# Kernel tuning notes

Hardware: AMD Instinct MI355X
Metric: run time of the kernel (lower is better)

## Reference

```python
import jax, jax.numpy as jnp
import numpy as np

N_SENT = 262144
N_BAGS = 4096
HIDDEN = 256
HIER = 2
LAYER0 = 14
NUM_CLASSES = 53


def setup_inputs() -> dict:
    key = jax.random.key(0)
    ks = jax.random.split(key, 8)
    x = jax.random.normal(ks[0], (N_SENT, HIDDEN), dtype=jnp.float32)
    rel_emb0 = jax.random.normal(ks[1], (LAYER0, HIDDEN), dtype=jnp.float32) * 0.1
    rel_emb1 = jax.random.normal(ks[2], (NUM_CLASSES, HIDDEN), dtype=jnp.float32) * 0.1
    disc = jax.random.normal(ks[3], (NUM_CLASSES, 2 * HIDDEN), dtype=jnp.float32) * 0.05
    bias = jnp.zeros((NUM_CLASSES,), dtype=jnp.float32)
    # relation_levels[r] = (coarse node id, fine node id) for relation r
    relation_levels = jnp.stack(
        [jax.random.randint(ks[4], (NUM_CLASSES,), 0, LAYER0, dtype=jnp.int32),
         jnp.arange(NUM_CLASSES, dtype=jnp.int32)], axis=1)
    label_index = jax.random.randint(ks[5], (N_SENT,), 0, NUM_CLASSES, dtype=jnp.int32)
    # ragged bag boundaries: scope[0]=0, scope[-1]=N_SENT, interior sorted
    interior = jnp.sort(jax.random.randint(ks[6], (N_BAGS - 1,), 1, N_SENT, dtype=jnp.int32))
    scope = jnp.concatenate([jnp.zeros((1,), jnp.int32), interior,
                             jnp.full((1,), N_SENT, jnp.int32)])
    return {"x": x, "rel_emb0": rel_emb0, "rel_emb1": rel_emb1, "disc": disc,
            "bias": bias, "relation_levels": relation_levels,
            "label_index": label_index, "scope": scope}


def _segment_ids(scope, n):
    # scope: [B+1] sorted boundaries -> per-sentence bag id [n]
    marks = jnp.zeros((n,), jnp.int32).at[scope[1:-1]].add(1)
    return jnp.cumsum(marks)


def reference(x, rel_emb0, rel_emb1, disc, bias, relation_levels, label_index, scope):
    n = x.shape[0]
    b = scope.shape[0] - 1
    seg = _segment_ids(scope, n)                       # [N]
    ll = relation_levels[label_index]                  # [N, 2]
    # per-level attention logits: <rel_emb[level][node], x>
    lg0 = jnp.sum(rel_emb0[ll[:, 0]] * x, axis=-1)     # [N]
    lg1 = jnp.sum(rel_emb1[ll[:, 1]] * x, axis=-1)     # [N]
    logits = jnp.stack([lg0, lg1], axis=1)             # [N, hier]
    # ragged softmax per bag (stable)
    m = jax.ops.segment_max(logits, seg, num_segments=b)     # [B, hier]
    e = jnp.exp(logits - m[seg])
    s = jax.ops.segment_sum(e, seg, num_segments=b)          # [B, hier]
    score = e / s[seg]                                       # [N, hier]
    # attention-weighted sentence reduction per bag per level
    weighted = score[:, :, None] * x[:, None, :]             # [N, hier, H]
    repre = jax.ops.segment_sum(weighted, seg, num_segments=b)  # [B, hier, H]
    stack_repre = repre.reshape(b, HIER * HIDDEN)            # [B, 2H]
    return stack_repre @ disc.T + bias                       # [B, 53]
```

## Files before the change

### kernel.cpp

```cpp
#include <hip/hip_runtime.h>
#include <math.h>

#define HIDDEN 256
#define NUM_CLASSES 53
#define NWAVES 4
#define BLOCK (NWAVES * 64)
#define KP 4

template <int CTRL>
__device__ __forceinline__ float dpp_add(float v) {
    int t = __builtin_amdgcn_update_dpp(0, __float_as_int(v), CTRL, 0xf, 0xf, true);
    return v + __int_as_float(t);
}

__device__ __forceinline__ float wave_sum64(float v) {
    v = dpp_add<0x111>(v);
    v = dpp_add<0x112>(v);
    v = dpp_add<0x114>(v);
    v = dpp_add<0x118>(v);
    v = dpp_add<0x142>(v);
    v = dpp_add<0x143>(v);
    return __int_as_float(__builtin_amdgcn_readlane(__float_as_int(v), 63));
}

__global__ __launch_bounds__(BLOCK, 4) void hattn_fused_kernel(
    const float* __restrict__ x,
    const float* __restrict__ rel_emb0,
    const float* __restrict__ rel_emb1,
    const float* __restrict__ disc,
    const float* __restrict__ bias,
    const int* __restrict__ relation_levels,
    const int* __restrict__ label_index,
    const int* __restrict__ scope,
    float* __restrict__ out)
{
    const int bag   = blockIdx.x;
    const int start = scope[bag];
    const int end   = scope[bag + 1];

    const int tid  = threadIdx.x;
    const int lane = tid & 63;
    const int wave = tid >> 6;
    const int col  = lane << 2;

    float4 o0 = make_float4(0,0,0,0), o1 = make_float4(0,0,0,0);
    float  l0 = 0.f, l1 = 0.f;

    for (int rbase = start + wave * KP; rbase < end; rbase += NWAVES * KP) {
        const int nv = end - rbase;

        float4 xv[KP];
        int    lbl[KP];
        #pragma unroll
        for (int k = 0; k < KP; ++k) {
            const int rc = (k < nv) ? (rbase + k) : rbase;
            const int rcs = __builtin_amdgcn_readfirstlane(rc);
            xv[k]  = *reinterpret_cast<const float4*>(x + ((size_t)rcs << 8) + col);
            lbl[k] = label_index[rcs];
        }

        float e0[KP], e1[KP];
        #pragma unroll
        for (int k = 0; k < KP; ++k) {
            const int2 rl = *reinterpret_cast<const int2*>(relation_levels + 2 * lbl[k]);
            const float4 r0 = *reinterpret_cast<const float4*>(rel_emb0 + ((size_t)rl.x << 8) + col);
            const float4 r1 = *reinterpret_cast<const float4*>(rel_emb1 + ((size_t)rl.y << 8) + col);
            float p0 = xv[k].x*r0.x + xv[k].y*r0.y + xv[k].z*r0.z + xv[k].w*r0.w;
            float p1 = xv[k].x*r1.x + xv[k].y*r1.y + xv[k].z*r1.z + xv[k].w*r1.w;
            const float s0 = wave_sum64(p0);
            const float s1 = wave_sum64(p1);
            e0[k] = (k < nv) ? __expf(s0) : 0.f;
            e1[k] = (k < nv) ? __expf(s1) : 0.f;
        }

        #pragma unroll
        for (int k = 0; k < KP; ++k) {
            l0 += e0[k];
            l1 += e1[k];
            o0.x += e0[k]*xv[k].x; o0.y += e0[k]*xv[k].y; o0.z += e0[k]*xv[k].z; o0.w += e0[k]*xv[k].w;
            o1.x += e1[k]*xv[k].x; o1.y += e1[k]*xv[k].y; o1.z += e1[k]*xv[k].z; o1.w += e1[k]*xv[k].w;
        }
    }

    __shared__ alignas(16) float s_o[2][NWAVES][HIDDEN];
    __shared__ float s_l[NWAVES][2];
    __shared__ alignas(16) float s_repre[2 * HIDDEN];
    __shared__ float s_inv[2];

    *reinterpret_cast<float4*>(&s_o[0][wave][col]) = o0;
    *reinterpret_cast<float4*>(&s_o[1][wave][col]) = o1;
    if (lane == 0) { s_l[wave][0] = l0; s_l[wave][1] = l1; }
    __syncthreads();

    {
        const int t = tid;
        const float a0 = s_o[0][0][t] + s_o[0][1][t] + s_o[0][2][t] + s_o[0][3][t];
        const float a1 = s_o[1][0][t] + s_o[1][1][t] + s_o[1][2][t] + s_o[1][3][t];
        s_repre[t]          = a0;
        s_repre[HIDDEN + t] = a1;
        if (tid == 0) {
            const float L0 = s_l[0][0] + s_l[1][0] + s_l[2][0] + s_l[3][0];
            const float L1 = s_l[0][1] + s_l[1][1] + s_l[2][1] + s_l[3][1];
            s_inv[0] = (L0 > 0.f) ? 1.f / L0 : 0.f;
            s_inv[1] = (L1 > 0.f) ? 1.f / L1 : 0.f;
        }
    }
    __syncthreads();

    {
        const int c  = tid >> 2;
        const int l4 = tid & 3;
        if (c < NUM_CLASSES) {
            const float4* dr = reinterpret_cast<const float4*>(disc + (size_t)c * (2 * HIDDEN));
            const float4* rp = reinterpret_cast<const float4*>(s_repre);
            float pH0 = 0.f, pH1 = 0.f;
            #pragma unroll
            for (int i = 0; i < 16; ++i) {
                const int idx = l4 + 4 * i;
                const float4 a = rp[idx];
                const float4 d = dr[idx];
                pH0 += a.x*d.x + a.y*d.y + a.z*d.z + a.w*d.w;
            }
            #pragma unroll
            for (int i = 16; i < 32; ++i) {
                const int idx = l4 + 4 * i;
                const float4 a = rp[idx];
                const float4 d = dr[idx];
                pH1 += a.x*d.x + a.y*d.y + a.z*d.z + a.w*d.w;
            }
            float p = pH0 * s_inv[0] + pH1 * s_inv[1];
            p = dpp_add<0xB1>(p);
            p = dpp_add<0x4E>(p);
            if (l4 == 0) out[bag * NUM_CLASSES + c] = p + bias[c];
        }
    }
}

extern "C" void kernel_launch(void* const* d_in, const int* in_sizes, int n_in,
                              void* d_out, int out_size, void* d_ws, size_t ws_size,
                              hipStream_t stream) {
    const float* x               = (const float*)d_in[0];
    const float* rel_emb0        = (const float*)d_in[1];
    const float* rel_emb1        = (const float*)d_in[2];
    const float* disc            = (const float*)d_in[3];
    const float* bias            = (const float*)d_in[4];
    const int*   relation_levels = (const int*)d_in[5];
    const int*   label_index     = (const int*)d_in[6];
    const int*   scope           = (const int*)d_in[7];
    float*       out             = (float*)d_out;

    const int n_bags = in_sizes[7] - 1;

    hattn_fused_kernel<<<n_bags, BLOCK, 0, stream>>>(
        x, rel_emb0, rel_emb1, disc, bias, relation_levels, label_index, scope, out);
}
```

Measured before the change: 419.9 us.

## Stage sentence tiles in LDS and split logit and reduction work across waves

Each block now copies 64-row tiles of x into padded shared memory. It computes both level logits per row with four threads and a short DPP reduction, instead of a full 64-lane reduction per row. The weighted sum is then split so each wave owns one level and half the rows, which removes the per-row wave-wide reductions. The cost is about 66KB of LDS per block, which cuts occupancy, plus three barriers per tile.

```diff
diff --git a/kernel.cpp b/kernel.cpp
--- a/kernel.cpp
+++ b/kernel.cpp
@@ -4,8 +4,9 @@
 #define HIDDEN 256
 #define NUM_CLASSES 53
 #define NWAVES 4
-#define BLOCK (NWAVES * 64)
-#define KP 4
+#define BLOCK 256
+#define TILE 64
+#define XPAD 260
 
 template <int CTRL>
 __device__ __forceinline__ float dpp_add(float v) {
@@ -13,17 +14,7 @@
     return v + __int_as_float(t);
 }
 
-__device__ __forceinline__ float wave_sum64(float v) {
-    v = dpp_add<0x111>(v);
-    v = dpp_add<0x112>(v);
-    v = dpp_add<0x114>(v);
-    v = dpp_add<0x118>(v);
-    v = dpp_add<0x142>(v);
-    v = dpp_add<0x143>(v);
-    return __int_as_float(__builtin_amdgcn_readlane(__float_as_int(v), 63));
-}
-
-__global__ __launch_bounds__(BLOCK, 4) void hattn_fused_kernel(
+__global__ __launch_bounds__(BLOCK, 2) void hattn_tile_kernel(
     const float* __restrict__ x,
     const float* __restrict__ rel_emb0,
     const float* __restrict__ rel_emb1,
@@ -34,105 +25,138 @@
     const int* __restrict__ scope,
     float* __restrict__ out)
 {
+    __shared__ alignas(16) float s_x[TILE][XPAD];
+    __shared__ alignas(16) float s_e0[TILE];
+    __shared__ alignas(16) float s_e1[TILE];
+    __shared__ int2  s_rl[NUM_CLASSES];
+    __shared__ int2  s_rlc[TILE];
+    __shared__ float s_lw[NWAVES];
+    __shared__ alignas(16) float s_rep2[2][2][HIDDEN];
+
+    const int tid  = threadIdx.x;
+    const int lane = tid & 63;
+    const int wave = tid >> 6;
+
+    if (tid < NUM_CLASSES)
+        s_rl[tid] = *reinterpret_cast<const int2*>(relation_levels + 2 * tid);
+    {
+        float4 z = make_float4(0.f, 0.f, 0.f, 0.f);
+        float* base = &s_x[0][0];
+        const int nf4 = (TILE * XPAD) / 4;
+        for (int i = tid; i < nf4; i += BLOCK)
+            *reinterpret_cast<float4*>(base + 4 * i) = z;
+    }
+
     const int bag   = blockIdx.x;
     const int start = scope[bag];
     const int end   = scope[bag + 1];
 
-    const int tid  = threadIdx.x;
-    const int lane = tid & 63;
-    const int wave = tid >> 6;
-    const int col  = lane << 2;
+    const int arow = tid >> 2;
+    const int q    = tid & 3;
 
-    float4 o0 = make_float4(0,0,0,0), o1 = make_float4(0,0,0,0);
-    float  l0 = 0.f, l1 = 0.f;
+    const int lvl     = wave >> 1;
+    const int rowhalf = wave & 1;
 
-    for (int rbase = start + wave * KP; rbase < end; rbase += NWAVES * KP) {
-        const int nv = end - rbase;
+    float4 oacc = make_float4(0.f, 0.f, 0.f, 0.f);
+    float  lacc = 0.f;
 
-        float4 xv[KP];
-        int    lbl[KP];
-        #pragma unroll
-        for (int k = 0; k < KP; ++k) {
-            const int rc = (k < nv) ? (rbase + k) : rbase;
-            const int rcs = __builtin_amdgcn_readfirstlane(rc);
-            xv[k]  = *reinterpret_cast<const float4*>(x + ((size_t)rcs << 8) + col);
-            lbl[k] = label_index[rcs];
+    __syncthreads();
+
+    for (int ts = start; ts < end; ts += TILE) {
+        #pragma unroll 4
+        for (int j = 0; j < 16; ++j) {
+            const int r  = 4 * j + wave;
+            const int rg = ts + r;
+            if (rg < end) {
+                const float4 v = *reinterpret_cast<const float4*>(
+                    x + ((size_t)rg << 8) + (lane << 2));
+                *reinterpret_cast<float4*>(&s_x[r][lane << 2]) = v;
+            }
         }
+        if (tid < TILE && ts + tid < end) {
+            const int lb = label_index[ts + tid];
+            s_rlc[tid] = s_rl[lb];
+        }
+        __syncthreads();
 
-        float e0[KP], e1[KP];
-        #pragma unroll
-        for (int k = 0; k < KP; ++k) {
-            const int2 rl = *reinterpret_cast<const int2*>(relation_levels + 2 * lbl[k]);
-            const float4 r0 = *reinterpret_cast<const float4*>(rel_emb0 + ((size_t)rl.x << 8) + col);
-            const float4 r1 = *reinterpret_cast<const float4*>(rel_emb1 + ((size_t)rl.y << 8) + col);
-            float p0 = xv[k].x*r0.x + xv[k].y*r0.y + xv[k].z*r0.z + xv[k].w*r0.w;
-            float p1 = xv[k].x*r1.x + xv[k].y*r1.y + xv[k].z*r1.z + xv[k].w*r1.w;
-            const float s0 = wave_sum64(p0);
-            const float s1 = wave_sum64(p1);
-            e0[k] = (k < nv) ? __expf(s0) : 0.f;
-            e1[k] = (k < nv) ? __expf(s1) : 0.f;
+        if (ts + arow < end) {
+            const int2 rl = s_rlc[arow];
+            const float* c0 = rel_emb0 + ((size_t)rl.x << 8) + (q << 6);
+            const float* c1 = rel_emb1 + ((size_t)rl.y << 8) + (q << 6);
+            const float* xr = &s_x[arow][q << 6];
+            float p0 = 0.f, p1 = 0.f;
+            #pragma unroll 4
+            for (int i = 0; i < 16; ++i) {
+                const float4 xv = *reinterpret_cast<const float4*>(xr + 4 * i);
+                const float4 a0 = *reinterpret_cast<const float4*>(c0 + 4 * i);
+                const float4 a1 = *reinterpret_cast<const float4*>(c1 + 4 * i);
+                p0 += xv.x*a0.x + xv.y*a0.y + xv.z*a0.z + xv.w*a0.w;
+                p1 += xv.x*a1.x + xv.y*a1.y + xv.z*a1.z + xv.w*a1.w;
+            }
+            p0 = dpp_add<0xB1>(p0); p0 = dpp_add<0x4E>(p0);
+            p1 = dpp_add<0xB1>(p1); p1 = dpp_add<0x4E>(p1);
+            if (q == 0) { s_e0[arow] = __expf(p0); s_e1[arow] = __expf(p1); }
+        } else if (q == 0) {
+            s_e0[arow] = 0.f; s_e1[arow] = 0.f;
         }
+        __syncthreads();
 
-        #pragma unroll
-        for (int k = 0; k < KP; ++k) {
-            l0 += e0[k];
-            l1 += e1[k];
-            o0.x += e0[k]*xv[k].x; o0.y += e0[k]*xv[k].y; o0.z += e0[k]*xv[k].z; o0.w += e0[k]*xv[k].w;
-            o1.x += e1[k]*xv[k].x; o1.y += e1[k]*xv[k].y; o1.z += e1[k]*xv[k].z; o1.w += e1[k]*xv[k].w;
+        {
+            const int   rbase = rowhalf << 5;
+            const float* eb   = lvl ? s_e1 : s_e0;
+            #pragma unroll
+            for (int g = 0; g < 8; ++g) {
+                const int r0 = rbase + 4 * g;
+                const float4 e4 = *reinterpret_cast<const float4*>(&eb[r0]);
+                #pragma unroll
+                for (int k = 0; k < 4; ++k) {
+                    const float e = (k == 0) ? e4.x : (k == 1) ? e4.y : (k == 2) ? e4.z : e4.w;
+                    const float4 xv = *reinterpret_cast<const float4*>(&s_x[r0 + k][lane << 2]);
+                    oacc.x += e * xv.x; oacc.y += e * xv.y;
+                    oacc.z += e * xv.z; oacc.w += e * xv.w;
+                    lacc += e;
+                }
+            }
         }
+        __syncthreads();
     }
 
-    __shared__ alignas(16) float s_o[2][NWAVES][HIDDEN];
-    __shared__ float s_l[NWAVES][2];
-    __shared__ alignas(16) float s_repre[2 * HIDDEN];
-    __shared__ float s_inv[2];
-
-    *reinterpret_cast<float4*>(&s_o[0][wave][col]) = o0;
-    *reinterpret_cast<float4*>(&s_o[1][wave][col]) = o1;
-    if (lane == 0) { s_l[wave][0] = l0; s_l[wave][1] = l1; }
+    *reinterpret_cast<float4*>(&s_rep2[lvl][rowhalf][lane << 2]) = oacc;
+    if (lane == 0) s_lw[wave] = lacc;
     __syncthreads();
 
-    {
-        const int t = tid;
-        const float a0 = s_o[0][0][t] + s_o[0][1][t] + s_o[0][2][t] + s_o[0][3][t];
-        const float a1 = s_o[1][0][t] + s_o[1][1][t] + s_o[1][2][t] + s_o[1][3][t];
-        s_repre[t]          = a0;
-        s_repre[HIDDEN + t] = a1;
-        if (tid == 0) {
-            const float L0 = s_l[0][0] + s_l[1][0] + s_l[2][0] + s_l[3][0];
-            const float L1 = s_l[0][1] + s_l[1][1] + s_l[2][1] + s_l[3][1];
-            s_inv[0] = (L0 > 0.f) ? 1.f / L0 : 0.f;
-            s_inv[1] = (L1 > 0.f) ? 1.f / L1 : 0.f;
+    const float L0 = s_lw[0] + s_lw[1];
+    const float L1 = s_lw[2] + s_lw[3];
+    const float i0 = (L0 > 0.f) ? 1.f / L0 : 0.f;
+    const float i1 = (L1 > 0.f) ? 1.f / L1 : 0.f;
+
+    const int c  = tid >> 2;
+    const int l4 = tid & 3;
+    if (c < NUM_CLASSES) {
+        const float4* dr  = reinterpret_cast<const float4*>(disc + (size_t)c * (2 * HIDDEN));
+        const float4* r00 = reinterpret_cast<const float4*>(&s_rep2[0][0][0]);
+        const float4* r01 = reinterpret_cast<const float4*>(&s_rep2[0][1][0]);
+        const float4* r10 = reinterpret_cast<const float4*>(&s_rep2[1][0][0]);
+        const float4* r11 = reinterpret_cast<const float4*>(&s_rep2[1][1][0]);
+        float pH0 = 0.f, pH1 = 0.f;
+        #pragma unroll
+        for (int i = 0; i < 16; ++i) {
+            const int idx = l4 + 4 * i;
+            const float4 a = r00[idx], b = r01[idx], d = dr[idx];
+            pH0 += (a.x + b.x) * d.x + (a.y + b.y) * d.y
+                 + (a.z + b.z) * d.z + (a.w + b.w) * d.w;
         }
-    }
-    __syncthreads();
-
-    {
-        const int c  = tid >> 2;
-        const int l4 = tid & 3;
-        if (c < NUM_CLASSES) {
-            const float4* dr = reinterpret_cast<const float4*>(disc + (size_t)c * (2 * HIDDEN));
-            const float4* rp = reinterpret_cast<const float4*>(s_repre);
-            float pH0 = 0.f, pH1 = 0.f;
-            #pragma unroll
-            for (int i = 0; i < 16; ++i) {
-                const int idx = l4 + 4 * i;
-                const float4 a = rp[idx];
-                const float4 d = dr[idx];
-                pH0 += a.x*d.x + a.y*d.y + a.z*d.z + a.w*d.w;
-            }
-            #pragma unroll
-            for (int i = 16; i < 32; ++i) {
-                const int idx = l4 + 4 * i;
-                const float4 a = rp[idx];
-                const float4 d = dr[idx];
-                pH1 += a.x*d.x + a.y*d.y + a.z*d.z + a.w*d.w;
-            }
-            float p = pH0 * s_inv[0] + pH1 * s_inv[1];
-            p = dpp_add<0xB1>(p);
-            p = dpp_add<0x4E>(p);
-            if (l4 == 0) out[bag * NUM_CLASSES + c] = p + bias[c];
+        #pragma unroll
+        for (int i = 0; i < 16; ++i) {
+            const int idx = l4 + 4 * i;
+            const float4 a = r10[idx], b = r11[idx], d = dr[64 + idx];
+            pH1 += (a.x + b.x) * d.x + (a.y + b.y) * d.y
+                 + (a.z + b.z) * d.z + (a.w + b.w) * d.w;
         }
+        float p = pH0 * i0 + pH1 * i1;
+        p = dpp_add<0xB1>(p);
+        p = dpp_add<0x4E>(p);
+        if (l4 == 0) out[bag * NUM_CLASSES + c] = p + bias[c];
     }
 }
 
@@ -151,6 +175,7 @@
 
     const int n_bags = in_sizes[7] - 1;
 
-    hattn_fused_kernel<<<n_bags, BLOCK, 0, stream>>>(
-        x, rel_emb0, rel_emb1, disc, bias, relation_levels, label_index, scope, out);
+    hattn_tile_kernel<<<n_bags, BLOCK, 0, stream>>>(
+        x, rel_emb0, rel_emb1, disc, bias,
+        relation_levels, label_index, scope, out);
 }
```

New measurement: 540.2 us. 1.29x slower.
